# Kernel optimization log

Measured on AMD Instinct MI355X. Metric: run time of the kernel, lower is better.

Reference implementation:

```python
import jax, jax.numpy as jnp
import numpy as np

KERNEL_LAM = 0.1


def setup_inputs() -> dict:
    key = jax.random.key(0)
    k1, k2, k3, k4 = jax.random.split(key, 4)
    B, H, L, C = 4, 1024, 4096, 1
    u = jax.random.normal(k1, (B, H, L), dtype=jnp.float32)
    kernel = jax.random.normal(k2, (C, H, 2 * L), dtype=jnp.float32) * 0.002
    D = jax.random.normal(k3, (C, H), dtype=jnp.float32)
    W = jax.random.normal(k4, (2 * H, C * H), dtype=jnp.float32) * (1.0 / np.sqrt(C * H))
    b = jnp.zeros((2 * H,), dtype=jnp.float32)
    return {"u": u, "kernel": kernel, "D": D, "W": W, "b": b}


def reference(u, kernel, D, W, b):
    B, H, L = u.shape
    n = 2 * L  # FFT length (kernel is length 2L)
    # soft-threshold the kernel
    k = jax.nn.relu(jnp.abs(kernel) - KERNEL_LAM) * jnp.sign(kernel)  # (C,H,2L)
    # FFT-based long convolution (flashfftconv equivalent): causal conv, take first L
    kf = jnp.fft.rfft(k, n=n)                       # (C,H,n//2+1)
    uf = jnp.fft.rfft(u, n=n)                       # (B,H,n//2+1)
    y = jnp.fft.irfft(uf[:, None] * kf[None], n=n)[..., :L]  # (B,C,H,L)
    # skip connection with D
    y = y + jnp.einsum('bhl,ch->bchl', u, D)
    # (B, C*H, L)
    y = y.reshape(B, -1, L)
    y = jax.nn.silu(y)
    # GLU projection over channel dim
    z = jnp.swapaxes(y, -1, -2) @ W.T + b           # (B,L,2H)
    a, g = jnp.split(z, 2, axis=-1)
    out = a * jax.nn.sigmoid(g)                     # (B,L,H)
    return jnp.swapaxes(out, -1, -2)                # (B,H,L)
```

## Files before the change

kernel.cpp:

```cpp
#include <hip/hip_runtime.h>
#include <stdint.h>

#define HD   1024
#define LD   4096
#define BATCH 4
#define KLEN 8192
#define LAM  0.1f
#define TAP_CAP 65536

typedef __attribute__((ext_vector_type(8))) short short8x;
typedef __attribute__((ext_vector_type(4))) float float4x;

struct Tap { int hd; float v; };

__device__ inline unsigned short f2bf(float x) {
    union { float f; uint32_t u; } v; v.f = x;
    uint32_t u = v.u;
    u += 0x7fffu + ((u >> 16) & 1u);
    return (unsigned short)(u >> 16);
}

__device__ inline void gload16(const void* g, void* l) {
    __builtin_amdgcn_global_load_lds(
        (const __attribute__((address_space(1))) void*)g,
        (__attribute__((address_space(3))) void*)l,
        16, 0, 0);
}

__device__ inline float silu_f(float x) { return x / (1.0f + __expf(-x)); }

__global__ void k_prep(const float* __restrict__ kern, int* __restrict__ ntaps,
                       Tap* __restrict__ taps,
                       const float* __restrict__ W, unsigned short* __restrict__ Wbf) {
    if (blockIdx.x < 1024) {
        int i = blockIdx.x * 256 + threadIdx.x;
        const float4* w4 = (const float4*)W;
        float4 a = w4[i * 2], b = w4[i * 2 + 1];
        short8x o;
        o[0] = (short)f2bf(a.x); o[1] = (short)f2bf(a.y);
        o[2] = (short)f2bf(a.z); o[3] = (short)f2bf(a.w);
        o[4] = (short)f2bf(b.x); o[5] = (short)f2bf(b.y);
        o[6] = (short)f2bf(b.z); o[7] = (short)f2bf(b.w);
        *(short8x*)(Wbf + (int64_t)i * 8) = o;
        return;
    }
    int bid = blockIdx.x - 1024;
    const float4* k4 = (const float4*)kern;
    int64_t total4 = (int64_t)HD * KLEN / 4;
    int64_t stride = (int64_t)2048 * 256;
    for (int64_t i = (int64_t)bid * 256 + threadIdx.x; i < total4; i += stride) {
        float4 v = k4[i];
        float vals[4] = {v.x, v.y, v.z, v.w};
#pragma unroll
        for (int j = 0; j < 4; j++) {
            float a = fabsf(vals[j]) - LAM;
            if (a > 0.0f) {
                int e = (int)(i * 4 + j);
                int slot = atomicAdd(ntaps, 1);
                if (slot < TAP_CAP) { taps[slot].hd = e; taps[slot].v = copysignf(a, vals[j]); }
            }
        }
    }
}

__global__ __launch_bounds__(256) void k_vt(const float* __restrict__ u,
                                            const float* __restrict__ Dv,
                                            const int* __restrict__ ntaps_p,
                                            const Tap* __restrict__ taps,
                                            unsigned short* __restrict__ Vt) {
    __shared__ float T[64 * 65];
    int nt = *ntaps_p;
    int lt = blockIdx.x * 64;
    int ht = blockIdx.y * 64;
    int b  = blockIdx.z;
    int tid = threadIdx.x;
    int lq = tid & 15;
    int hh = tid >> 4;
#pragma unroll
    for (int r = 0; r < 4; r++) {
        int h = hh + r * 16;
        int hg = ht + h;
        int64_t base = ((int64_t)b * HD + hg) * LD + lt + lq * 4;
        float4 v = *(const float4*)(u + base);
        float d = Dv[hg];
        v.x *= d; v.y *= d; v.z *= d; v.w *= d;
        if (nt != 0) {
            int ncl = min(nt, TAP_CAP);
            float acc[4] = {v.x, v.y, v.z, v.w};
            const float* ub = u + ((int64_t)b * HD + hg) * LD;
            for (int j = 0; j < ncl; j++) {
                int hd = taps[j].hd;
                if ((hd >> 13) != hg) continue;
                int dly = hd & (KLEN - 1);
#pragma unroll
                for (int e = 0; e < 4; e++) {
                    int t = lt + lq * 4 + e;
                    int s = t - dly;
                    if (s < 0) s += KLEN;
                    if (s < LD) acc[e] += taps[j].v * ub[s];
                }
            }
            v.x = acc[0]; v.y = acc[1]; v.z = acc[2]; v.w = acc[3];
        }
        int p = h * 65 + lq * 4;
        T[p]     = silu_f(v.x);
        T[p + 1] = silu_f(v.y);
        T[p + 2] = silu_f(v.z);
        T[p + 3] = silu_f(v.w);
    }
    __syncthreads();
    int h8 = (tid & 7) * 8;
    int nb = tid >> 3;
#pragma unroll
    for (int p = 0; p < 2; p++) {
        int nl = nb + p * 32;
        short8x o;
#pragma unroll
        for (int j = 0; j < 8; j++) o[j] = (short)f2bf(T[(h8 + j) * 65 + nl]);
        int64_t n = (int64_t)b * LD + lt + nl;
        *(short8x*)(Vt + n * HD + ht + h8) = o;
    }
}

__global__ __launch_bounds__(256, 2) void k_gemm(const unsigned short* __restrict__ Wbf,
                                                 const unsigned short* __restrict__ Vt,
                                                 const float* __restrict__ bvec,
                                                 float* __restrict__ out) {
    __shared__ unsigned short smem[24576];
    int m0 = blockIdx.x * 128;
    int n0 = blockIdx.y * 128;
    int tid = threadIdx.x;

    const unsigned short* gsrc[12];
    unsigned short* ldst[12];
#pragma unroll
    for (int i = 0; i < 12; i++) {
        int c = tid + i * 256;
        ldst[i] = smem + c * 8;
        if (c < 2048) {
            int r = c >> 3, s = c & 7;
            int kg = s ^ (r & 7);
            int grow = (r < 128) ? (m0 + r) : (1024 + m0 + (r - 128));
            gsrc[i] = Wbf + (int64_t)grow * HD + kg * 8;
        } else {
            int cc = c - 2048;
            int col = cc >> 3, s = cc & 7;
            int kg = s ^ (col & 7);
            gsrc[i] = Vt + (int64_t)(n0 + col) * HD + kg * 8;
        }
    }

    int lane = tid & 63;
    int wid  = tid >> 6;
    int wm = wid >> 1, wn = wid & 1;
    int l15 = lane & 15, quad = lane >> 4;
    int xr = l15 & 7;

    int rba[4], rbg[4], rbb[4];
#pragma unroll
    for (int i = 0; i < 4; i++) {
        int ra = wm * 64 + i * 16 + l15;
        rba[i] = ra * 64;
        rbg[i] = (128 + ra) * 64;
        int cb = wn * 64 + i * 16 + l15;
        rbb[i] = 16384 + cb * 64;
    }

    float4x acca[4][4], accg[4][4];
#pragma unroll
    for (int i = 0; i < 4; i++)
#pragma unroll
        for (int j = 0; j < 4; j++) {
            acca[i][j] = (float4x){0.f, 0.f, 0.f, 0.f};
            accg[i][j] = (float4x){0.f, 0.f, 0.f, 0.f};
        }

    for (int kt = 0; kt < 16; kt++) {
#pragma unroll
        for (int i = 0; i < 12; i++) gload16(gsrc[i], ldst[i]);
#pragma unroll
        for (int i = 0; i < 12; i++) gsrc[i] += 64;
        __syncthreads();
#pragma unroll
        for (int ks = 0; ks < 2; ks++) {
            int off = ((ks * 4 + quad) ^ xr) * 8;
            short8x af[4], gf[4], bf[4];
#pragma unroll
            for (int i = 0; i < 4; i++) {
                af[i] = *(const short8x*)(smem + rba[i] + off);
                gf[i] = *(const short8x*)(smem + rbg[i] + off);
                bf[i] = *(const short8x*)(smem + rbb[i] + off);
            }
#pragma unroll
            for (int i = 0; i < 4; i++)
#pragma unroll
                for (int j = 0; j < 4; j++) {
                    acca[i][j] = __builtin_amdgcn_mfma_f32_16x16x32_bf16(af[i], bf[j], acca[i][j], 0, 0, 0);
                    accg[i][j] = __builtin_amdgcn_mfma_f32_16x16x32_bf16(gf[i], bf[j], accg[i][j], 0, 0, 0);
                }
        }
        __syncthreads();
    }

    int b = n0 >> 12;
#pragma unroll
    for (int i = 0; i < 4; i++) {
        int h = m0 + wm * 64 + i * 16 + quad * 4;
        float ba[4], bg[4];
#pragma unroll
        for (int r = 0; r < 4; r++) { ba[r] = bvec[h + r]; bg[r] = bvec[1024 + h + r]; }
#pragma unroll
        for (int j = 0; j < 4; j++) {
            int n = n0 + wn * 64 + j * 16 + l15;
            int l = n & (LD - 1);
            float* op = out + ((int64_t)b * HD + h) * LD + l;
#pragma unroll
            for (int r = 0; r < 4; r++) {
                float av = acca[i][j][r] + ba[r];
                float gv = accg[i][j][r] + bg[r];
                op[(int64_t)r * LD] = av / (1.0f + __expf(-gv));
            }
        }
    }
}

extern "C" void kernel_launch(void* const* d_in, const int* in_sizes, int n_in,
                              void* d_out, int out_size, void* d_ws, size_t ws_size,
                              hipStream_t stream) {
    const float* u    = (const float*)d_in[0];
    const float* kern = (const float*)d_in[1];
    const float* Dv   = (const float*)d_in[2];
    const float* W    = (const float*)d_in[3];
    const float* bv   = (const float*)d_in[4];
    float* out = (float*)d_out;

    char* ws = (char*)d_ws;
    int* ntaps = (int*)ws;
    Tap* taps  = (Tap*)(ws + 256);
    unsigned short* Wbf = (unsigned short*)(ws + (1 << 20));
    unsigned short* Vt  = (unsigned short*)(ws + (8 << 20));

    hipMemsetAsync(ntaps, 0, 256, stream);
    hipLaunchKernelGGL(k_prep, dim3(3072),      dim3(256), 0, stream, kern, ntaps, taps, W, Wbf);
    hipLaunchKernelGGL(k_vt,   dim3(64, 16, 4), dim3(256), 0, stream, u, Dv, ntaps, taps, Vt);
    hipLaunchKernelGGL(k_gemm, dim3(8, 128),    dim3(256), 0, stream, Wbf, Vt, bv, out);
}
```

Measured before the change: 219.7 us.

## Double-buffer GLU GEMM with 128x256 tiles, swizzled grid and MFMA priority

Restructures the bf16 GLU GEMM to use 512-thread blocks computing 128x256 output tiles. Global-to-LDS loads are double-buffered, using explicit vmcnt waits and barriers so the next K-slice loads while the current one is computed. Block indices are swizzled for L2 locality, and s_setprio is raised around MFMA bursts, with gate-fragment loads split to lower register pressure. The 128KB of LDS limits occupancy to one block per CU, and the hand-written waitcnt sequence is fragile.

```diff
diff --git a/kernel.cpp b/kernel.cpp
--- a/kernel.cpp
+++ b/kernel.cpp
@@ -7,6 +7,7 @@
 #define KLEN 8192
 #define LAM  0.1f
 #define TAP_CAP 65536
+#define NT   16
 
 typedef __attribute__((ext_vector_type(8))) short short8x;
 typedef __attribute__((ext_vector_type(4))) float float4x;
@@ -122,21 +123,21 @@
     }
 }
 
-__global__ __launch_bounds__(256, 2) void k_gemm(const unsigned short* __restrict__ Wbf,
+__global__ __launch_bounds__(512, 2) void k_gemm(const unsigned short* __restrict__ Wbf,
                                                  const unsigned short* __restrict__ Vt,
                                                  const float* __restrict__ bvec,
                                                  float* __restrict__ out) {
-    __shared__ unsigned short smem[24576];
-    int m0 = blockIdx.x * 128;
-    int n0 = blockIdx.y * 128;
-    int tid = threadIdx.x;
-
-    const unsigned short* gsrc[12];
-    unsigned short* ldst[12];
-#pragma unroll
-    for (int i = 0; i < 12; i++) {
-        int c = tid + i * 256;
-        ldst[i] = smem + c * 8;
+    __shared__ unsigned short smem[65536];
+    int tid  = threadIdx.x;
+    int flat = blockIdx.x;
+    int swz  = (flat & 7) * 64 + (flat >> 3);
+    int m0   = (swz & 7) * 128;
+    int n0   = (swz >> 3) * 256;
+
+    const unsigned short* gsrc[8];
+#pragma unroll
+    for (int i = 0; i < 8; i++) {
+        int c = tid + i * 512;
         if (c < 2048) {
             int r = c >> 3, s = c & 7;
             int kg = s ^ (r & 7);
@@ -152,7 +153,7 @@
 
     int lane = tid & 63;
     int wid  = tid >> 6;
-    int wm = wid >> 1, wn = wid & 1;
+    int wm = wid >> 2, wn = wid & 3;
     int l15 = lane & 15, quad = lane >> 4;
     int xr = l15 & 7;
 
@@ -175,32 +176,63 @@
             accg[i][j] = (float4x){0.f, 0.f, 0.f, 0.f};
         }
 
-    for (int kt = 0; kt < 16; kt++) {
-#pragma unroll
-        for (int i = 0; i < 12; i++) gload16(gsrc[i], ldst[i]);
-#pragma unroll
-        for (int i = 0; i < 12; i++) gsrc[i] += 64;
-        __syncthreads();
+    auto stage = [&](int buf) {
+        unsigned short* lb = smem + buf * 32768;
+#pragma unroll
+        for (int i = 0; i < 8; i++) {
+            gload16(gsrc[i], lb + (tid + i * 512) * 8);
+            gsrc[i] += 64;
+        }
+    };
+
+    auto compute = [&](int buf) {
+        const unsigned short* sb = smem + buf * 32768;
 #pragma unroll
         for (int ks = 0; ks < 2; ks++) {
             int off = ((ks * 4 + quad) ^ xr) * 8;
-            short8x af[4], gf[4], bf[4];
+            short8x af[4], bfr[4];
 #pragma unroll
             for (int i = 0; i < 4; i++) {
-                af[i] = *(const short8x*)(smem + rba[i] + off);
-                gf[i] = *(const short8x*)(smem + rbg[i] + off);
-                bf[i] = *(const short8x*)(smem + rbb[i] + off);
-            }
+                af[i]  = *(const short8x*)(sb + rba[i] + off);
+                bfr[i] = *(const short8x*)(sb + rbb[i] + off);
+            }
+            __builtin_amdgcn_s_setprio(1);
 #pragma unroll
             for (int i = 0; i < 4; i++)
 #pragma unroll
-                for (int j = 0; j < 4; j++) {
-                    acca[i][j] = __builtin_amdgcn_mfma_f32_16x16x32_bf16(af[i], bf[j], acca[i][j], 0, 0, 0);
-                    accg[i][j] = __builtin_amdgcn_mfma_f32_16x16x32_bf16(gf[i], bf[j], accg[i][j], 0, 0, 0);
-                }
-        }
-        __syncthreads();
-    }
+                for (int j = 0; j < 4; j++)
+                    acca[i][j] = __builtin_amdgcn_mfma_f32_16x16x32_bf16(af[i], bfr[j], acca[i][j], 0, 0, 0);
+            __builtin_amdgcn_s_setprio(0);
+            short8x gf[4];
+#pragma unroll
+            for (int i = 0; i < 4; i++)
+                gf[i] = *(const short8x*)(sb + rbg[i] + off);
+            __builtin_amdgcn_s_setprio(1);
+#pragma unroll
+            for (int i = 0; i < 4; i++)
+#pragma unroll
+                for (int j = 0; j < 4; j++)
+                    accg[i][j] = __builtin_amdgcn_mfma_f32_16x16x32_bf16(gf[i], bfr[j], accg[i][j], 0, 0, 0);
+            __builtin_amdgcn_s_setprio(0);
+        }
+    };
+
+    stage(0);
+    stage(1);
+    for (int t = 0; t < NT - 2; t++) {
+        asm volatile("s_waitcnt vmcnt(8)" ::: "memory");
+        asm volatile("s_barrier" ::: "memory");
+        compute(t & 1);
+        asm volatile("s_waitcnt lgkmcnt(0)" ::: "memory");
+        asm volatile("s_barrier" ::: "memory");
+        stage(t & 1);
+    }
+    asm volatile("s_waitcnt vmcnt(8)" ::: "memory");
+    asm volatile("s_barrier" ::: "memory");
+    compute(0);
+    asm volatile("s_waitcnt vmcnt(0)" ::: "memory");
+    asm volatile("s_barrier" ::: "memory");
+    compute(1);
 
     int b = n0 >> 12;
 #pragma unroll
@@ -243,5 +275,5 @@
     hipMemsetAsync(ntaps, 0, 256, stream);
     hipLaunchKernelGGL(k_prep, dim3(3072),      dim3(256), 0, stream, kern, ntaps, taps, W, Wbf);
     hipLaunchKernelGGL(k_vt,   dim3(64, 16, 4), dim3(256), 0, stream, u, Dv, ntaps, taps, Vt);
-    hipLaunchKernelGGL(k_gemm, dim3(8, 128),    dim3(256), 0, stream, Wbf, Vt, bv, out);
-}
+    hipLaunchKernelGGL(k_gemm, dim3(512),       dim3(512), 0, stream, Wbf, Vt, bv, out);
+}
```

New measurement: 220.0 us. No clear change (+0.1%).

## Rewrite GEMM as 512-thread double-buffered ping-pong pipeline with swizzled block order

Applied to the files above, without the earlier changes.

The GLU GEMM kernel moves to 512-thread blocks computing 128x256 output tiles. LDS is double-buffered, and per-chunk global-to-LDS async loads are interleaved with MFMA phases, using explicit vmcnt waits, barriers and setprio, so loads overlap compute. A swizzled 1D grid order is added to improve L2 reuse. The fine-grained barrier schedule adds synchronisation overhead and correctness risk, and the larger LDS footprint may limit occupancy.

```diff
diff --git a/kernel.cpp b/kernel.cpp
--- a/kernel.cpp
+++ b/kernel.cpp
@@ -7,6 +7,7 @@
 #define KLEN 8192
 #define LAM  0.1f
 #define TAP_CAP 65536
+#define NT   16
 
 typedef __attribute__((ext_vector_type(8))) short short8x;
 typedef __attribute__((ext_vector_type(4))) float float4x;
@@ -122,37 +123,60 @@
     }
 }
 
-__global__ __launch_bounds__(256, 2) void k_gemm(const unsigned short* __restrict__ Wbf,
+#define BAR       asm volatile("s_barrier" ::: "memory")
+#define WAITV2    asm volatile("s_waitcnt vmcnt(2)" ::: "memory")
+#define WAITV0    asm volatile("s_waitcnt vmcnt(0)" ::: "memory")
+
+#define STAGE(srcarr, buf, regionOff, kt) do {                                 \
+    unsigned short* lb_ = smem + (buf) * 32768 + (regionOff);                  \
+    gload16(srcarr[0] + (kt) * 64, lb_ + tid * 8);                             \
+    gload16(srcarr[1] + (kt) * 64, lb_ + (tid + 512) * 8);                     \
+} while (0)
+
+#define LDFR(sb, rb, off, dst) do {                                            \
+    _Pragma("unroll")                                                          \
+    for (int _i = 0; _i < 4; _i++)                                             \
+        dst[_i] = *(const short8x*)((sb) + rb[_i] + (off));                    \
+} while (0)
+
+#define MMA(afr, br, acc) do {                                                 \
+    __builtin_amdgcn_s_setprio(1);                                             \
+    _Pragma("unroll")                                                          \
+    for (int _i = 0; _i < 4; _i++)                                             \
+        _Pragma("unroll")                                                      \
+        for (int _j = 0; _j < 4; _j++)                                         \
+            acc[_i][_j] = __builtin_amdgcn_mfma_f32_16x16x32_bf16(             \
+                afr[_i], br[_j], acc[_i][_j], 0, 0, 0);                        \
+    __builtin_amdgcn_s_setprio(0);                                             \
+} while (0)
+
+__global__ __launch_bounds__(512, 2) void k_gemm(const unsigned short* __restrict__ Wbf,
                                                  const unsigned short* __restrict__ Vt,
                                                  const float* __restrict__ bvec,
                                                  float* __restrict__ out) {
-    __shared__ unsigned short smem[24576];
-    int m0 = blockIdx.x * 128;
-    int n0 = blockIdx.y * 128;
-    int tid = threadIdx.x;
-
-    const unsigned short* gsrc[12];
-    unsigned short* ldst[12];
-#pragma unroll
-    for (int i = 0; i < 12; i++) {
-        int c = tid + i * 256;
-        ldst[i] = smem + c * 8;
-        if (c < 2048) {
-            int r = c >> 3, s = c & 7;
-            int kg = s ^ (r & 7);
-            int grow = (r < 128) ? (m0 + r) : (1024 + m0 + (r - 128));
-            gsrc[i] = Wbf + (int64_t)grow * HD + kg * 8;
-        } else {
-            int cc = c - 2048;
-            int col = cc >> 3, s = cc & 7;
-            int kg = s ^ (col & 7);
-            gsrc[i] = Vt + (int64_t)(n0 + col) * HD + kg * 8;
-        }
+    __shared__ unsigned short smem[65536];
+    int tid  = threadIdx.x;
+    int flat = blockIdx.x;
+    int swz  = (flat & 7) * 64 + (flat >> 3);
+    int m0   = (swz & 7) * 128;
+    int n0   = (swz >> 3) * 256;
+
+    const unsigned short* sA0[2]; const unsigned short* sA1[2];
+    const unsigned short* sB0[2]; const unsigned short* sB1[2];
+#pragma unroll
+    for (int j = 0; j < 2; j++) {
+        int c = tid + j * 512;
+        int r = c >> 3, s = c & 7;
+        int kg = s ^ (r & 7);
+        sA0[j] = Wbf + (int64_t)(m0 + r) * HD + kg * 8;
+        sA1[j] = Wbf + (int64_t)(1024 + m0 + r) * HD + kg * 8;
+        sB0[j] = Vt + (int64_t)(n0 + r) * HD + kg * 8;
+        sB1[j] = Vt + (int64_t)(n0 + 128 + r) * HD + kg * 8;
     }
 
     int lane = tid & 63;
     int wid  = tid >> 6;
-    int wm = wid >> 1, wn = wid & 1;
+    int wm = wid >> 2, wn = wid & 3;
     int l15 = lane & 15, quad = lane >> 4;
     int xr = l15 & 7;
 
@@ -165,6 +189,11 @@
         int cb = wn * 64 + i * 16 + l15;
         rbb[i] = 16384 + cb * 64;
     }
+    int off0 = (quad ^ xr) * 8;
+    int off1 = ((4 + quad) ^ xr) * 8;
+
+    const unsigned short* sb0 = smem;
+    const unsigned short* sb1 = smem + 32768;
 
     float4x acca[4][4], accg[4][4];
 #pragma unroll
@@ -175,31 +204,60 @@
             accg[i][j] = (float4x){0.f, 0.f, 0.f, 0.f};
         }
 
-    for (int kt = 0; kt < 16; kt++) {
-#pragma unroll
-        for (int i = 0; i < 12; i++) gload16(gsrc[i], ldst[i]);
-#pragma unroll
-        for (int i = 0; i < 12; i++) gsrc[i] += 64;
-        __syncthreads();
-#pragma unroll
-        for (int ks = 0; ks < 2; ks++) {
-            int off = ((ks * 4 + quad) ^ xr) * 8;
-            short8x af[4], gf[4], bf[4];
-#pragma unroll
-            for (int i = 0; i < 4; i++) {
-                af[i] = *(const short8x*)(smem + rba[i] + off);
-                gf[i] = *(const short8x*)(smem + rbg[i] + off);
-                bf[i] = *(const short8x*)(smem + rbb[i] + off);
-            }
-#pragma unroll
-            for (int i = 0; i < 4; i++)
-#pragma unroll
-                for (int j = 0; j < 4; j++) {
-                    acca[i][j] = __builtin_amdgcn_mfma_f32_16x16x32_bf16(af[i], bf[j], acca[i][j], 0, 0, 0);
-                    accg[i][j] = __builtin_amdgcn_mfma_f32_16x16x32_bf16(gf[i], bf[j], accg[i][j], 0, 0, 0);
-                }
-        }
-        __syncthreads();
+    short8x fr[4], b0r[4], b1r[4];
+
+    STAGE(sA0, 0, 0, 0); STAGE(sA1, 0, 8192, 0);
+    STAGE(sB0, 0, 16384, 0); STAGE(sB1, 0, 24576, 0);
+    STAGE(sA0, 1, 0, 1);
+    WAITV2; BAR;
+
+    for (int i = 0; i < 7; i++) {
+        int t1 = 2 * i + 1, tn0 = 2 * i + 2, tn1 = 2 * i + 3;
+        LDFR(sb0, rbg, off0, fr); LDFR(sb0, rbb, off0, b0r);
+        STAGE(sA1, 1, 8192, t1); STAGE(sB0, 1, 16384, t1);
+        BAR; MMA(fr, b0r, accg); BAR;
+        LDFR(sb0, rbg, off1, fr); LDFR(sb0, rbb, off1, b1r);
+        STAGE(sB1, 1, 24576, t1);
+        BAR; MMA(fr, b1r, accg); BAR;
+        LDFR(sb0, rba, off0, fr);
+        STAGE(sA1, 0, 8192, tn0);
+        BAR; MMA(fr, b0r, acca); BAR;
+        LDFR(sb0, rba, off1, fr);
+        WAITV2;
+        BAR; MMA(fr, b1r, acca); BAR;
+        LDFR(sb1, rba, off0, fr); LDFR(sb1, rbb, off0, b0r);
+        STAGE(sA0, 0, 0, tn0);
+        BAR; MMA(fr, b0r, acca); BAR;
+        LDFR(sb1, rba, off1, fr); LDFR(sb1, rbb, off1, b1r);
+        STAGE(sB0, 0, 16384, tn0); STAGE(sB1, 0, 24576, tn0);
+        BAR; MMA(fr, b1r, acca); BAR;
+        LDFR(sb1, rbg, off0, fr);
+        STAGE(sA0, 1, 0, tn1);
+        BAR; MMA(fr, b0r, accg); BAR;
+        LDFR(sb1, rbg, off1, fr);
+        WAITV2;
+        BAR; MMA(fr, b1r, accg); BAR;
+    }
+    {
+        LDFR(sb0, rbg, off0, fr); LDFR(sb0, rbb, off0, b0r);
+        STAGE(sA1, 1, 8192, 15); STAGE(sB0, 1, 16384, 15);
+        BAR; MMA(fr, b0r, accg); BAR;
+        LDFR(sb0, rbg, off1, fr); LDFR(sb0, rbb, off1, b1r);
+        STAGE(sB1, 1, 24576, 15);
+        BAR; MMA(fr, b1r, accg); BAR;
+        LDFR(sb0, rba, off0, fr);
+        BAR; MMA(fr, b0r, acca); BAR;
+        LDFR(sb0, rba, off1, fr);
+        WAITV0;
+        BAR; MMA(fr, b1r, acca); BAR;
+        LDFR(sb1, rba, off0, fr); LDFR(sb1, rbb, off0, b0r);
+        BAR; MMA(fr, b0r, acca); BAR;
+        LDFR(sb1, rba, off1, fr); LDFR(sb1, rbb, off1, b1r);
+        BAR; MMA(fr, b1r, acca); BAR;
+        LDFR(sb1, rbg, off0, fr);
+        BAR; MMA(fr, b0r, accg); BAR;
+        LDFR(sb1, rbg, off1, fr);
+        MMA(fr, b1r, accg);
     }
 
     int b = n0 >> 12;
@@ -243,5 +301,5 @@
     hipMemsetAsync(ntaps, 0, 256, stream);
     hipLaunchKernelGGL(k_prep, dim3(3072),      dim3(256), 0, stream, kern, ntaps, taps, W, Wbf);
     hipLaunchKernelGGL(k_vt,   dim3(64, 16, 4), dim3(256), 0, stream, u, Dv, ntaps, taps, Vt);
-    hipLaunchKernelGGL(k_gemm, dim3(8, 128),    dim3(256), 0, stream, Wbf, Vt, bv, out);
-}
+    hipLaunchKernelGGL(k_gemm, dim3(512),       dim3(512), 0, stream, Wbf, Vt, bv, out);
+}
```

New measurement: 221.8 us. No clear change (+0.9%).
